# Kernel optimization log

Measured on AMD Instinct MI355X. Metric: run time of the kernel, lower is better.

## Reference

```python
import jax, jax.numpy as jnp
import numpy as np

TAU = 2.0
BN_EPS = 1e-5


def ms_lif(x_seq, v_th):
    # Multi-step LIF: v <- v + (x - v)/tau; spike = H(v - v_th); hard reset to 0.
    def step(v, x):
        v = v + (x - v) / TAU
        s = (v >= v_th).astype(x.dtype)
        v = v * (1.0 - s)
        return v, s
    _, spikes = jax.lax.scan(step, jnp.zeros_like(x_seq[0]), x_seq)
    return spikes


def conv1x1(x, w):
    # x: [TB, C, H, W], w: [O, C]
    return jnp.einsum('bchw,oc->bohw', x, w)


def bn(x, gamma, beta, mean, var):
    scale = gamma / jnp.sqrt(var + BN_EPS)
    shift = beta - mean * scale
    return x * scale[None, :, None, None] + shift[None, :, None, None]


def setup_inputs() -> dict:
    key = jax.random.key(0)
    ks = jax.random.split(key, 20)
    T, B, C, H, W = 4, 32, 384, 16, 16
    d = {'x': jax.random.normal(ks[0], (T, B, C, H, W), jnp.float32)}
    def bn_params(i):
        return (jax.random.uniform(ks[i], (C,), jnp.float32, 0.5, 1.5),
                jax.random.normal(ks[i + 1], (C,), jnp.float32) * 0.1,
                jax.random.normal(ks[i + 2], (C,), jnp.float32) * 0.1,
                jax.random.uniform(ks[i + 3], (C,), jnp.float32, 0.5, 1.5))
    d['q_w'] = jax.random.normal(ks[1], (C, C), jnp.float32) * (C ** -0.5)
    d['q_gamma'], d['q_beta'], d['q_mean'], d['q_var'] = bn_params(2)
    d['k_w'] = jax.random.normal(ks[6], (C, C), jnp.float32) * (C ** -0.5)
    d['k_gamma'], d['k_beta'], d['k_mean'], d['k_var'] = bn_params(7)
    d['v_w'] = jax.random.normal(ks[11], (C, C), jnp.float32) * (C ** -0.5)
    d['v_gamma'], d['v_beta'], d['v_mean'], d['v_var'] = bn_params(12)
    d['proj_w'] = jax.random.normal(ks[16], (C, C), jnp.float32) * (C ** -0.5)
    d['proj_b'] = jnp.zeros((C,), jnp.float32)
    d['proj_gamma'], d['proj_beta'], d['proj_mean'], d['proj_var'] = bn_params(16)
    return d


def reference(x, q_w, q_gamma, q_beta, q_mean, q_var,
              k_w, k_gamma, k_beta, k_mean, k_var,
              v_w, v_gamma, v_beta, v_mean, v_var,
              proj_w, proj_b, proj_gamma, proj_beta, proj_mean, proj_var):
    T, B, C, H, W = x.shape
    nh = 8
    dh = C // nh
    N = H * W
    identity = x
    xs = ms_lif(x, 1.0)                        # shortcut_lif
    xf = xs.reshape(T * B, C, H, W)

    def branch(w, g, b, m, v_):
        y = bn(conv1x1(xf, w), g, b, m, v_).reshape(T, B, C, H, W)
        return ms_lif(y, 1.0)

    def to_heads(s):  # [T,B,C,H,W] -> [T,B,nh,N,dh]
        return s.reshape(T, B, C, N).transpose(0, 1, 3, 2).reshape(T, B, N, nh, dh).transpose(0, 1, 3, 2, 4)

    q = to_heads(branch(q_w, q_gamma, q_beta, q_mean, q_var))
    k = to_heads(branch(k_w, k_gamma, k_beta, k_mean, k_var))
    v = to_heads(branch(v_w, v_gamma, v_beta, v_mean, v_var))

    kv = (k * v).sum(axis=-2, keepdims=True)   # [T,B,nh,1,dh]
    kv = ms_lif(kv, 0.5)                       # talking_heads_lif (v_th=0.5)
    y = q * kv                                 # [T,B,nh,N,dh]
    y = y.transpose(0, 1, 2, 4, 3).reshape(T * B, C, H, W)
    out = conv1x1(y, proj_w) + proj_b[None, :, None, None]
    out = bn(out, proj_gamma, proj_beta, proj_mean, proj_var).reshape(T, B, C, H, W)
    out = out + identity
    return out, v
```

## Files before the change

### kernel.cpp

```cpp
#include <hip/hip_runtime.h>

#define T_ 4
#define B_ 32
#define C_ 384
#define N_ 256
#define NH_ 8
#define DH_ 48
#define CG_ 48
#define WELE_ 147456
#define FRAGS_M_ 442368
#define ELEMS_ ((size_t)T_*B_*C_*N_)

typedef __bf16 bf16x8 __attribute__((ext_vector_type(8)));
typedef float  f32x4  __attribute__((ext_vector_type(4)));
typedef unsigned int u32x4 __attribute__((ext_vector_type(4)));
typedef unsigned int u32x2 __attribute__((ext_vector_type(2)));
typedef unsigned short u16;

__device__ __forceinline__ float bf2f(u16 h){
  unsigned u = ((unsigned)h) << 16;
  return __builtin_bit_cast(float, u);
}
__device__ __forceinline__ u16 f2bf(float f){
  unsigned u = __builtin_bit_cast(unsigned, f);
  u += 0x7FFFu + ((u >> 16) & 1u);
  return (u16)(u >> 16);
}

__global__ __launch_bounds__(256) void k0_split(
    const float* __restrict__ wq, const float* __restrict__ wk,
    const float* __restrict__ wv, const float* __restrict__ wp,
    u16* __restrict__ ws)
{
  const int m = blockIdx.y;
  const int tid = blockIdx.x * 256 + threadIdx.x;
  const float* W = (m == 0) ? wq : (m == 1) ? wk : (m == 2) ? wv : wp;
  const int fo   = tid / 768;
  const int rem  = tid % 768;
  const int k32  = rem / 64;
  const int lane = rem % 64;
  const int row  = fo*16 + (lane & 15);
  const int col  = k32*32 + (lane >> 4)*8;
  const float* src = W + (size_t)row*C_ + col;

  u16 hi8[8], mi8[8], lo8[8];
#pragma unroll
  for (int e = 0; e < 8; e++){
    float w = src[e];
    u16 hi = f2bf(w);  float r1 = w  - bf2f(hi);
    u16 mi = f2bf(r1); float r2 = r1 - bf2f(mi);
    u16 lo = f2bf(r2);
    hi8[e] = hi; mi8[e] = mi; lo8[e] = lo;
  }
  u16* dst = ws + (size_t)m*FRAGS_M_ + (size_t)((fo*12 + k32)*3)*512 + (size_t)lane*8;
  u32x4 pk;
#pragma unroll
  for (int p = 0; p < 3; p++){
    const u16* s = (p == 0) ? hi8 : (p == 1) ? mi8 : lo8;
    pk[0] = (unsigned)s[0] | ((unsigned)s[1] << 16);
    pk[1] = (unsigned)s[2] | ((unsigned)s[3] << 16);
    pk[2] = (unsigned)s[4] | ((unsigned)s[5] << 16);
    pk[3] = (unsigned)s[6] | ((unsigned)s[7] << 16);
    *(u32x4*)(dst + (size_t)p*512) = pk;
  }
}

__global__ __launch_bounds__(256) void k1_lif_in(const float* __restrict__ x, u16* __restrict__ xs)
{
  const int b = blockIdx.x, cg = blockIdx.y, n = threadIdx.x;
  const int c0 = cg * 8;
  float v[8];
#pragma unroll
  for (int i = 0; i < 8; i++) v[i] = 0.f;
#pragma unroll
  for (int t = 0; t < T_; t++){
    const float* xp = x + (((size_t)(t*B_ + b))*C_ + c0)*N_ + n;
    u16 sp[8];
#pragma unroll
    for (int i = 0; i < 8; i++){
      float xv = xp[(size_t)i * N_];
      float vv = v[i] + (xv - v[i]) * 0.5f;
      bool s = vv >= 1.0f;
      sp[i] = s ? (u16)0x3F80u : (u16)0u;
      v[i] = s ? 0.f : vv;
    }
    u32x4 pk;
    pk[0] = (unsigned)sp[0] | ((unsigned)sp[1] << 16);
    pk[1] = (unsigned)sp[2] | ((unsigned)sp[3] << 16);
    pk[2] = (unsigned)sp[4] | ((unsigned)sp[5] << 16);
    pk[3] = (unsigned)sp[6] | ((unsigned)sp[7] << 16);
    *(u32x4*)(xs + ((size_t)((t*B_ + b)*CG_ + cg))*2048 + (size_t)n*8) = pk;
  }
}

__global__ __launch_bounds__(256) void k2_branch(
    const u16* __restrict__ xs, const u16* __restrict__ wsplit,
    const float* __restrict__ gq, const float* __restrict__ beq, const float* __restrict__ mq, const float* __restrict__ vaq,
    const float* __restrict__ gk, const float* __restrict__ bek, const float* __restrict__ mk, const float* __restrict__ vak,
    const float* __restrict__ gv, const float* __restrict__ bev, const float* __restrict__ mv, const float* __restrict__ vav,
    u16* __restrict__ qspk, u16* __restrict__ kspk, u16* __restrict__ vspk)
{
  const int id   = blockIdx.x;
  const int xcd  = id & 7;
  const int rest = id >> 3;
  const int obi  = rest % 18;
  const int nb4  = (rest / 18) & 3;
  const int bloc = rest / 72;
  const int b    = xcd * 4 + bloc;
  const int ob   = obi * 64;
  const int nb   = nb4 * 64;

  const int lane = threadIdx.x & 63;
  const int w = threadIdx.x >> 6;
  const int wo = w & 1, wn = w >> 1;
  const int l15 = lane & 15, lg = lane >> 4;
  const int branch = ob / C_;
  const int obr = (ob % C_) + wo * 32;
  const int fo  = obr >> 4;

  const float *G, *Be, *M, *Va; u16* spdst;
  if (branch == 0){ G=gq; Be=beq; M=mq; Va=vaq; spdst=qspk; }
  else if (branch == 1){ G=gk; Be=bek; M=mk; Va=vak; spdst=kspk; }
  else { G=gv; Be=bev; M=mv; Va=vav; spdst=vspk; }

  const u16* Wb = wsplit + (size_t)branch*FRAGS_M_ + (size_t)lane*8;
  const int nbl = nb + wn * 32;

  const u16* xbt[T_];
#pragma unroll
  for (int t = 0; t < T_; t++)
    xbt[t] = xs + ((size_t)((t*B_ + b)*CG_) + lg)*2048 + (size_t)(nbl + l15)*8;

  f32x4 acc[T_][2][2];
#pragma unroll
  for (int t = 0; t < T_; t++)
#pragma unroll
    for (int io = 0; io < 2; io++)
#pragma unroll
      for (int in = 0; in < 2; in++) acc[t][io][in] = (f32x4){0.f,0.f,0.f,0.f};

  for (int k = 0; k < 12; k++){
    bf16x8 wf[2][3];
#pragma unroll
    for (int io = 0; io < 2; io++)
#pragma unroll
      for (int p = 0; p < 3; p++)
        wf[io][p] = *(const bf16x8*)(Wb + (size_t)(((fo + io)*12 + k)*3 + p)*512);

#pragma unroll
    for (int t = 0; t < T_; t++){
      bf16x8 bb[2];
#pragma unroll
      for (int in = 0; in < 2; in++)
        bb[in] = *(const bf16x8*)(xbt[t] + (size_t)k*8192 + in*128);
#pragma unroll
      for (int in = 0; in < 2; in++){
        acc[t][0][in] = __builtin_amdgcn_mfma_f32_16x16x32_bf16(wf[0][2], bb[in], acc[t][0][in], 0, 0, 0);
        acc[t][0][in] = __builtin_amdgcn_mfma_f32_16x16x32_bf16(wf[0][1], bb[in], acc[t][0][in], 0, 0, 0);
        acc[t][0][in] = __builtin_amdgcn_mfma_f32_16x16x32_bf16(wf[0][0], bb[in], acc[t][0][in], 0, 0, 0);
        acc[t][1][in] = __builtin_amdgcn_mfma_f32_16x16x32_bf16(wf[1][2], bb[in], acc[t][1][in], 0, 0, 0);
        acc[t][1][in] = __builtin_amdgcn_mfma_f32_16x16x32_bf16(wf[1][1], bb[in], acc[t][1][in], 0, 0, 0);
        acc[t][1][in] = __builtin_amdgcn_mfma_f32_16x16x32_bf16(wf[1][0], bb[in], acc[t][1][in], 0, 0, 0);
      }
    }
  }

  float sc[2][4], sh[2][4];
#pragma unroll
  for (int io = 0; io < 2; io++)
#pragma unroll
    for (int j = 0; j < 4; j++){
      int o = obr + io*16 + lg*4 + j;
      float s = G[o] / sqrtf(Va[o] + 1e-5f);
      sc[io][j] = s;
      sh[io][j] = Be[o] - __fmul_rn(M[o], s);
    }

  float vm[2][2][4];
#pragma unroll
  for (int io = 0; io < 2; io++)
#pragma unroll
    for (int in = 0; in < 2; in++)
#pragma unroll
      for (int j = 0; j < 4; j++) vm[io][in][j] = 0.f;

#pragma unroll
  for (int t = 0; t < T_; t++){
#pragma unroll
    for (int io = 0; io < 2; io++)
#pragma unroll
      for (int in = 0; in < 2; in++){
        int n = nbl + in*16 + l15;
        u16 sp[4];
#pragma unroll
        for (int j = 0; j < 4; j++){
          float z = __fadd_rn(__fmul_rn(acc[t][io][in][j], sc[io][j]), sh[io][j]);
          float vv = vm[io][in][j];
          vv = vv + (z - vv) * 0.5f;
          bool s = vv >= 1.0f;
          sp[j] = s ? (u16)0x3F80u : (u16)0u;
          vm[io][in][j] = s ? 0.f : vv;
        }
        u32x2 pk;
        pk[0] = (unsigned)sp[0] | ((unsigned)sp[1] << 16);
        pk[1] = (unsigned)sp[2] | ((unsigned)sp[3] << 16);
        int od = obr + io*16 + lg*4;
        u16* dst = spdst + (size_t)((t*B_ + b)*CG_ + (od >> 3))*2048 + (size_t)n*8 + (od & 7);
        *(u32x2*)dst = pk;
      }
  }
}

__global__ __launch_bounds__(256) void k3_kv(
    const u16* __restrict__ kspk, const u16* __restrict__ vspk, u16* __restrict__ kvm)
{
  const int wid  = (int)((blockIdx.x * blockDim.x + threadIdx.x) >> 6);
  const int lane = threadIdx.x & 63;
  const int b = wid / CG_, cg = wid % CG_;
  float u[8];
#pragma unroll
  for (int i = 0; i < 8; i++) u[i] = 0.f;

#pragma unroll
  for (int t = 0; t < T_; t++){
    int cnt[8];
#pragma unroll
    for (int i = 0; i < 8; i++) cnt[i] = 0;
    const size_t rowoff = (size_t)((t*B_ + b)*CG_ + cg)*2048;
    const u16* kp = kspk + rowoff;
    const u16* vp = vspk + rowoff;
#pragma unroll
    for (int j = 0; j < 4; j++){
      int n = j*64 + lane;
      u32x4 kk = *(const u32x4*)(kp + (size_t)n*8);
      u32x4 vv = *(const u32x4*)(vp + (size_t)n*8);
#pragma unroll
      for (int wd = 0; wd < 4; wd++){
        unsigned both = kk[wd] & vv[wd];
        cnt[2*wd]   += (both & 0xFFFFu) ? 1 : 0;
        cnt[2*wd+1] += (both >> 16)     ? 1 : 0;
      }
    }
#pragma unroll
    for (int i = 0; i < 8; i++){
#pragma unroll
      for (int off = 32; off >= 1; off >>= 1) cnt[i] += __shfl_xor(cnt[i], off, 64);
    }
    u16 mk[8];
#pragma unroll
    for (int i = 0; i < 8; i++){
      float kvf = (float)cnt[i];
      float uu = u[i] + (kvf - u[i]) * 0.5f;
      bool s = uu >= 0.5f;
      mk[i] = s ? (u16)0xFFFFu : (u16)0u;
      u[i] = s ? 0.f : uu;
    }
    if (lane == 0){
      u32x4 pk;
      pk[0] = (unsigned)mk[0] | ((unsigned)mk[1] << 16);
      pk[1] = (unsigned)mk[2] | ((unsigned)mk[3] << 16);
      pk[2] = (unsigned)mk[4] | ((unsigned)mk[5] << 16);
      pk[3] = (unsigned)mk[6] | ((unsigned)mk[7] << 16);
      *(u32x4*)(kvm + (size_t)(t*B_ + b)*C_ + cg*8) = pk;
    }
  }
}

__global__ __launch_bounds__(256) void k5_vtrans(const u16* __restrict__ vspk, float* __restrict__ vout)
{
  const int tb = blockIdx.x, h = blockIdx.y;
  const u16* src = vspk + ((size_t)tb*CG_ + h*6)*2048;
  float* dst = vout + ((size_t)tb*NH_ + h)*(N_*DH_);
#pragma unroll
  for (int i = 0; i < 12; i++){
    int f = i*1024 + threadIdx.x*4;
    int n = f / DH_;
    int d = f - n*DH_;
    u32x2 rv = *(const u32x2*)(src + (size_t)(d >> 3)*2048 + (size_t)n*8 + (d & 7));
    f32x4 o;
    o[0] = (rv[0] & 0xFFFFu) ? 1.f : 0.f;
    o[1] = (rv[0] >> 16)     ? 1.f : 0.f;
    o[2] = (rv[1] & 0xFFFFu) ? 1.f : 0.f;
    o[3] = (rv[1] >> 16)     ? 1.f : 0.f;
    *(f32x4*)(dst + f) = o;
  }
}

__global__ __launch_bounds__(256) void k4_proj(
    const u16* __restrict__ qspk, const u16* __restrict__ kvm, const u16* __restrict__ wsplit,
    const float* __restrict__ pb,
    const float* __restrict__ gp, const float* __restrict__ bep,
    const float* __restrict__ mp, const float* __restrict__ vap,
    const float* __restrict__ x, float* __restrict__ out)
{
  const int id   = blockIdx.x;
  const int xcd  = id & 7;
  const int rest = id >> 3;
  const int obi  = rest % 6;
  const int nb2  = (rest / 6) & 1;
  const int tbl  = rest / 12;
  const int tb   = xcd * 16 + tbl;
  const int ob   = obi * 64;
  const int nb   = nb2 * 128;

  __shared__ __align__(16) u16 kvmask[C_];
  for (int i = threadIdx.x; i < C_; i += 256) kvmask[i] = kvm[(size_t)tb*C_ + i];
  __syncthreads();

  const int lane = threadIdx.x & 63;
  const int w = threadIdx.x >> 6;
  const int wo = w & 1, wn = w >> 1;
  const int l15 = lane & 15, lg = lane >> 4;
  const int obw = ob + wo * 32;
  const int fo  = obw >> 4;
  const int nbl = nb + wn * 64;

  const u16* Wp = wsplit + (size_t)3*FRAGS_M_ + (size_t)lane*8;

  float sc[2][4], sh[2][4], pbv[2][4];
#pragma unroll
  for (int io = 0; io < 2; io++)
#pragma unroll
    for (int j = 0; j < 4; j++){
      int o = obw + io*16 + lg*4 + j;
      float s = gp[o] / sqrtf(vap[o] + 1e-5f);
      sc[io][j] = s;
      sh[io][j] = bep[o] - __fmul_rn(mp[o], s);
      pbv[io][j] = pb[o];
    }

  f32x4 acc[2][4];
#pragma unroll
  for (int io = 0; io < 2; io++)
#pragma unroll
    for (int in = 0; in < 4; in++) acc[io][in] = (f32x4){0.f,0.f,0.f,0.f};

  const u16* qb = qspk + ((size_t)(tb*CG_) + lg)*2048 + (size_t)(nbl + l15)*8;

  for (int k = 0; k < 12; k++){
    bf16x8 a0 = *(const bf16x8*)(Wp + (size_t)(((fo    )*12 + k)*3)*512);
    bf16x8 a1 = *(const bf16x8*)(Wp + (size_t)(((fo + 1)*12 + k)*3)*512);
    u32x4 mv = *(const u32x4*)&kvmask[k*32 + lg*8];
    bf16x8 bb[4];
#pragma unroll
    for (int in = 0; in < 4; in++){
      u32x4 qv = *(const u32x4*)(qb + (size_t)k*8192 + in*128);
      u32x4 yv = qv & mv;
      bb[in] = __builtin_bit_cast(bf16x8, yv);
    }
#pragma unroll
    for (int in = 0; in < 4; in++){
      acc[0][in] = __builtin_amdgcn_mfma_f32_16x16x32_bf16(a0, bb[in], acc[0][in], 0, 0, 0);
      acc[1][in] = __builtin_amdgcn_mfma_f32_16x16x32_bf16(a1, bb[in], acc[1][in], 0, 0, 0);
    }
  }

#pragma unroll
  for (int io = 0; io < 2; io++)
#pragma unroll
    for (int in = 0; in < 4; in++){
      int n = nbl + in*16 + l15;
#pragma unroll
      for (int j = 0; j < 4; j++){
        int o = obw + io*16 + lg*4 + j;
        size_t off = ((size_t)tb*C_ + o)*N_ + n;
        float z = __fadd_rn(acc[io][in][j], pbv[io][j]);
        z = __fmul_rn(z, sc[io][j]);
        z = __fadd_rn(z, sh[io][j]);
        z = __fadd_rn(z, x[off]);
        out[off] = z;
      }
    }
}

extern "C" void kernel_launch(void* const* d_in, const int* in_sizes, int n_in,
                              void* d_out, int out_size, void* d_ws, size_t ws_size,
                              hipStream_t stream)
{
  (void)in_sizes; (void)n_in; (void)out_size; (void)ws_size;
  const float* x   = (const float*)d_in[0];
  const float* qw  = (const float*)d_in[1];
  const float* qg  = (const float*)d_in[2];
  const float* qbe = (const float*)d_in[3];
  const float* qm  = (const float*)d_in[4];
  const float* qva = (const float*)d_in[5];
  const float* kw  = (const float*)d_in[6];
  const float* kg  = (const float*)d_in[7];
  const float* kbe = (const float*)d_in[8];
  const float* km  = (const float*)d_in[9];
  const float* kva = (const float*)d_in[10];
  const float* vw  = (const float*)d_in[11];
  const float* vg  = (const float*)d_in[12];
  const float* vbe = (const float*)d_in[13];
  const float* vm  = (const float*)d_in[14];
  const float* vva = (const float*)d_in[15];
  const float* pw  = (const float*)d_in[16];
  const float* pb  = (const float*)d_in[17];
  const float* pg  = (const float*)d_in[18];
  const float* pbe = (const float*)d_in[19];
  const float* pm  = (const float*)d_in[20];
  const float* pva = (const float*)d_in[21];

  float* out  = (float*)d_out;
  float* vout = out + ELEMS_;

  u16* vspk = (u16*)d_out;

  u16* wsplit = (u16*)d_ws;
  u16* xs   = wsplit + (size_t)4*FRAGS_M_;
  u16* qspk = xs   + ELEMS_;
  u16* kspk = qspk + ELEMS_;
  u16* kvm  = kspk + ELEMS_;

  k0_split<<<dim3(72, 4), 256, 0, stream>>>(qw, kw, vw, pw, wsplit);
  k1_lif_in<<<dim3(B_, CG_), 256, 0, stream>>>(x, xs);
  k2_branch<<<dim3(2304), 256, 0, stream>>>(xs, wsplit,
      qg, qbe, qm, qva,
      kg, kbe, km, kva,
      vg, vbe, vm, vva,
      qspk, kspk, vspk);
  k3_kv<<<dim3(384), 256, 0, stream>>>(kspk, vspk, kvm);
  k5_vtrans<<<dim3(T_*B_, NH_), 256, 0, stream>>>(vspk, vout);
  k4_proj<<<dim3(1536), 256, 0, stream>>>(qspk, kvm, wsplit,
      pb, pg, pbe, pm, pva, x, out);
}
```

Measured before the change: 141.7 us.

## Switch QKV and projection GEMMs to 32x32x16 MFMA tiles

Replaces the 16x16x32 bf16 MFMA tiling with 32x32x16 instructions in the fused QKV conv+BN+LIF kernel and the projection kernel. The weight-splitting kernel writes fragments in the new 32-row layout. Each wave now issues fewer, larger MFMAs and loads fewer activation fragments per K step, which cuts instruction and load overhead. The accumulator register layout changes, so the epilogue index math for BN, LIF and output stores is rewritten, and there is some risk of index errors or different memory access patterns.

```diff
diff --git a/kernel.cpp b/kernel.cpp
--- a/kernel.cpp
+++ b/kernel.cpp
@@ -13,6 +13,7 @@
 
 typedef __bf16 bf16x8 __attribute__((ext_vector_type(8)));
 typedef float  f32x4  __attribute__((ext_vector_type(4)));
+typedef float  f32x16 __attribute__((ext_vector_type(16)));
 typedef unsigned int u32x4 __attribute__((ext_vector_type(4)));
 typedef unsigned int u32x2 __attribute__((ext_vector_type(2)));
 typedef unsigned short u16;
@@ -35,12 +36,12 @@
   const int m = blockIdx.y;
   const int tid = blockIdx.x * 256 + threadIdx.x;
   const float* W = (m == 0) ? wq : (m == 1) ? wk : (m == 2) ? wv : wp;
-  const int fo   = tid / 768;
-  const int rem  = tid % 768;
-  const int k32  = rem / 64;
+  const int fo   = tid / 1536;
+  const int rem  = tid % 1536;
+  const int k16  = rem / 64;
   const int lane = rem % 64;
-  const int row  = fo*16 + (lane & 15);
-  const int col  = k32*32 + (lane >> 4)*8;
+  const int row  = fo*32 + (lane & 31);
+  const int col  = k16*16 + (lane >> 5)*8;
   const float* src = W + (size_t)row*C_ + col;
 
   u16 hi8[8], mi8[8], lo8[8];
@@ -52,7 +53,7 @@
     u16 lo = f2bf(r2);
     hi8[e] = hi; mi8[e] = mi; lo8[e] = lo;
   }
-  u16* dst = ws + (size_t)m*FRAGS_M_ + (size_t)((fo*12 + k32)*3)*512 + (size_t)lane*8;
+  u16* dst = ws + (size_t)m*FRAGS_M_ + (size_t)((fo*24 + k16)*3)*512 + (size_t)lane*8;
   u32x4 pk;
 #pragma unroll
   for (int p = 0; p < 3; p++){
@@ -113,10 +114,10 @@
   const int lane = threadIdx.x & 63;
   const int w = threadIdx.x >> 6;
   const int wo = w & 1, wn = w >> 1;
-  const int l15 = lane & 15, lg = lane >> 4;
+  const int l31 = lane & 31, hi = lane >> 5;
   const int branch = ob / C_;
   const int obr = (ob % C_) + wo * 32;
-  const int fo  = obr >> 4;
+  const int fo  = obr >> 5;
 
   const float *G, *Be, *M, *Va; u16* spdst;
   if (branch == 0){ G=gq; Be=beq; M=mq; Va=vaq; spdst=qspk; }
@@ -125,89 +126,73 @@
 
   const u16* Wb = wsplit + (size_t)branch*FRAGS_M_ + (size_t)lane*8;
   const int nbl = nb + wn * 32;
+  const int n   = nbl + l31;
 
   const u16* xbt[T_];
 #pragma unroll
   for (int t = 0; t < T_; t++)
-    xbt[t] = xs + ((size_t)((t*B_ + b)*CG_) + lg)*2048 + (size_t)(nbl + l15)*8;
-
-  f32x4 acc[T_][2][2];
+    xbt[t] = xs + ((size_t)((t*B_ + b)*CG_) + hi)*2048 + (size_t)n*8;
+
+  f32x16 acc[T_];
 #pragma unroll
   for (int t = 0; t < T_; t++)
 #pragma unroll
-    for (int io = 0; io < 2; io++)
-#pragma unroll
-      for (int in = 0; in < 2; in++) acc[t][io][in] = (f32x4){0.f,0.f,0.f,0.f};
-
-  for (int k = 0; k < 12; k++){
-    bf16x8 wf[2][3];
-#pragma unroll
-    for (int io = 0; io < 2; io++)
-#pragma unroll
-      for (int p = 0; p < 3; p++)
-        wf[io][p] = *(const bf16x8*)(Wb + (size_t)(((fo + io)*12 + k)*3 + p)*512);
+    for (int r = 0; r < 16; r++) acc[t][r] = 0.f;
+
+  for (int k = 0; k < 24; k++){
+    bf16x8 wf[3];
+#pragma unroll
+    for (int p = 0; p < 3; p++)
+      wf[p] = *(const bf16x8*)(Wb + (size_t)((fo*24 + k)*3 + p)*512);
+
+    bf16x8 bb[T_];
+#pragma unroll
+    for (int t = 0; t < T_; t++)
+      bb[t] = *(const bf16x8*)(xbt[t] + (size_t)k*4096);
 
 #pragma unroll
     for (int t = 0; t < T_; t++){
-      bf16x8 bb[2];
-#pragma unroll
-      for (int in = 0; in < 2; in++)
-        bb[in] = *(const bf16x8*)(xbt[t] + (size_t)k*8192 + in*128);
-#pragma unroll
-      for (int in = 0; in < 2; in++){
-        acc[t][0][in] = __builtin_amdgcn_mfma_f32_16x16x32_bf16(wf[0][2], bb[in], acc[t][0][in], 0, 0, 0);
-        acc[t][0][in] = __builtin_amdgcn_mfma_f32_16x16x32_bf16(wf[0][1], bb[in], acc[t][0][in], 0, 0, 0);
-        acc[t][0][in] = __builtin_amdgcn_mfma_f32_16x16x32_bf16(wf[0][0], bb[in], acc[t][0][in], 0, 0, 0);
-        acc[t][1][in] = __builtin_amdgcn_mfma_f32_16x16x32_bf16(wf[1][2], bb[in], acc[t][1][in], 0, 0, 0);
-        acc[t][1][in] = __builtin_amdgcn_mfma_f32_16x16x32_bf16(wf[1][1], bb[in], acc[t][1][in], 0, 0, 0);
-        acc[t][1][in] = __builtin_amdgcn_mfma_f32_16x16x32_bf16(wf[1][0], bb[in], acc[t][1][in], 0, 0, 0);
+      acc[t] = __builtin_amdgcn_mfma_f32_32x32x16_bf16(wf[2], bb[t], acc[t], 0, 0, 0);
+      acc[t] = __builtin_amdgcn_mfma_f32_32x32x16_bf16(wf[1], bb[t], acc[t], 0, 0, 0);
+      acc[t] = __builtin_amdgcn_mfma_f32_32x32x16_bf16(wf[0], bb[t], acc[t], 0, 0, 0);
+    }
+  }
+
+  float sc[16], sh[16];
+#pragma unroll
+  for (int r = 0; r < 16; r++){
+    int o = obr + (r & 3) + 8*(r >> 2) + 4*hi;
+    float s = G[o] / sqrtf(Va[o] + 1e-5f);
+    sc[r] = s;
+    sh[r] = Be[o] - __fmul_rn(M[o], s);
+  }
+
+  float vmr[16];
+#pragma unroll
+  for (int r = 0; r < 16; r++) vmr[r] = 0.f;
+
+#pragma unroll
+  for (int t = 0; t < T_; t++){
+#pragma unroll
+    for (int g = 0; g < 4; g++){
+      u16 sp[4];
+#pragma unroll
+      for (int j = 0; j < 4; j++){
+        int r = g*4 + j;
+        float z = __fadd_rn(__fmul_rn(acc[t][r], sc[r]), sh[r]);
+        float vv = vmr[r];
+        vv = vv + (z - vv) * 0.5f;
+        bool s = vv >= 1.0f;
+        sp[j] = s ? (u16)0x3F80u : (u16)0u;
+        vmr[r] = s ? 0.f : vv;
       }
-    }
-  }
-
-  float sc[2][4], sh[2][4];
-#pragma unroll
-  for (int io = 0; io < 2; io++)
-#pragma unroll
-    for (int j = 0; j < 4; j++){
-      int o = obr + io*16 + lg*4 + j;
-      float s = G[o] / sqrtf(Va[o] + 1e-5f);
-      sc[io][j] = s;
-      sh[io][j] = Be[o] - __fmul_rn(M[o], s);
-    }
-
-  float vm[2][2][4];
-#pragma unroll
-  for (int io = 0; io < 2; io++)
-#pragma unroll
-    for (int in = 0; in < 2; in++)
-#pragma unroll
-      for (int j = 0; j < 4; j++) vm[io][in][j] = 0.f;
-
-#pragma unroll
-  for (int t = 0; t < T_; t++){
-#pragma unroll
-    for (int io = 0; io < 2; io++)
-#pragma unroll
-      for (int in = 0; in < 2; in++){
-        int n = nbl + in*16 + l15;
-        u16 sp[4];
-#pragma unroll
-        for (int j = 0; j < 4; j++){
-          float z = __fadd_rn(__fmul_rn(acc[t][io][in][j], sc[io][j]), sh[io][j]);
-          float vv = vm[io][in][j];
-          vv = vv + (z - vv) * 0.5f;
-          bool s = vv >= 1.0f;
-          sp[j] = s ? (u16)0x3F80u : (u16)0u;
-          vm[io][in][j] = s ? 0.f : vv;
-        }
-        u32x2 pk;
-        pk[0] = (unsigned)sp[0] | ((unsigned)sp[1] << 16);
-        pk[1] = (unsigned)sp[2] | ((unsigned)sp[3] << 16);
-        int od = obr + io*16 + lg*4;
-        u16* dst = spdst + (size_t)((t*B_ + b)*CG_ + (od >> 3))*2048 + (size_t)n*8 + (od & 7);
-        *(u32x2*)dst = pk;
-      }
+      u32x2 pk;
+      pk[0] = (unsigned)sp[0] | ((unsigned)sp[1] << 16);
+      pk[1] = (unsigned)sp[2] | ((unsigned)sp[3] << 16);
+      int od = obr + 8*g + 4*hi;
+      u16* dst = spdst + (size_t)((t*B_ + b)*CG_ + (od >> 3))*2048 + (size_t)n*8 + (od & 7);
+      *(u32x2*)dst = pk;
+    }
   }
 }
 
@@ -310,67 +295,57 @@
   const int lane = threadIdx.x & 63;
   const int w = threadIdx.x >> 6;
   const int wo = w & 1, wn = w >> 1;
-  const int l15 = lane & 15, lg = lane >> 4;
-  const int obw = ob + wo * 32;
-  const int fo  = obw >> 4;
+  const int l31 = lane & 31, hi = lane >> 5;
+  const int ow  = ob + wo * 32;
+  const int fo  = ow >> 5;
   const int nbl = nb + wn * 64;
 
   const u16* Wp = wsplit + (size_t)3*FRAGS_M_ + (size_t)lane*8;
 
-  float sc[2][4], sh[2][4], pbv[2][4];
-#pragma unroll
-  for (int io = 0; io < 2; io++)
-#pragma unroll
-    for (int j = 0; j < 4; j++){
-      int o = obw + io*16 + lg*4 + j;
-      float s = gp[o] / sqrtf(vap[o] + 1e-5f);
-      sc[io][j] = s;
-      sh[io][j] = bep[o] - __fmul_rn(mp[o], s);
-      pbv[io][j] = pb[o];
-    }
-
-  f32x4 acc[2][4];
-#pragma unroll
-  for (int io = 0; io < 2; io++)
-#pragma unroll
-    for (int in = 0; in < 4; in++) acc[io][in] = (f32x4){0.f,0.f,0.f,0.f};
-
-  const u16* qb = qspk + ((size_t)(tb*CG_) + lg)*2048 + (size_t)(nbl + l15)*8;
-
-  for (int k = 0; k < 12; k++){
-    bf16x8 a0 = *(const bf16x8*)(Wp + (size_t)(((fo    )*12 + k)*3)*512);
-    bf16x8 a1 = *(const bf16x8*)(Wp + (size_t)(((fo + 1)*12 + k)*3)*512);
-    u32x4 mv = *(const u32x4*)&kvmask[k*32 + lg*8];
-    bf16x8 bb[4];
-#pragma unroll
-    for (int in = 0; in < 4; in++){
-      u32x4 qv = *(const u32x4*)(qb + (size_t)k*8192 + in*128);
+  float sc[16], sh[16], pbv[16];
+#pragma unroll
+  for (int r = 0; r < 16; r++){
+    int o = ow + (r & 3) + 8*(r >> 2) + 4*hi;
+    float s = gp[o] / sqrtf(vap[o] + 1e-5f);
+    sc[r] = s;
+    sh[r] = bep[o] - __fmul_rn(mp[o], s);
+    pbv[r] = pb[o];
+  }
+
+  f32x16 acc[2];
+#pragma unroll
+  for (int in = 0; in < 2; in++)
+#pragma unroll
+    for (int r = 0; r < 16; r++) acc[in][r] = 0.f;
+
+  const u16* qb = qspk + ((size_t)(tb*CG_) + hi)*2048 + (size_t)(nbl + l31)*8;
+
+  for (int k = 0; k < 24; k++){
+    bf16x8 a = *(const bf16x8*)(Wp + (size_t)((fo*24 + k)*3)*512);
+    u32x4 mv = *(const u32x4*)&kvmask[k*16 + hi*8];
+#pragma unroll
+    for (int in = 0; in < 2; in++){
+      u32x4 qv = *(const u32x4*)(qb + (size_t)k*4096 + in*256);
       u32x4 yv = qv & mv;
-      bb[in] = __builtin_bit_cast(bf16x8, yv);
-    }
-#pragma unroll
-    for (int in = 0; in < 4; in++){
-      acc[0][in] = __builtin_amdgcn_mfma_f32_16x16x32_bf16(a0, bb[in], acc[0][in], 0, 0, 0);
-      acc[1][in] = __builtin_amdgcn_mfma_f32_16x16x32_bf16(a1, bb[in], acc[1][in], 0, 0, 0);
-    }
-  }
-
-#pragma unroll
-  for (int io = 0; io < 2; io++)
-#pragma unroll
-    for (int in = 0; in < 4; in++){
-      int n = nbl + in*16 + l15;
-#pragma unroll
-      for (int j = 0; j < 4; j++){
-        int o = obw + io*16 + lg*4 + j;
-        size_t off = ((size_t)tb*C_ + o)*N_ + n;
-        float z = __fadd_rn(acc[io][in][j], pbv[io][j]);
-        z = __fmul_rn(z, sc[io][j]);
-        z = __fadd_rn(z, sh[io][j]);
-        z = __fadd_rn(z, x[off]);
-        out[off] = z;
-      }
-    }
+      bf16x8 bbv = __builtin_bit_cast(bf16x8, yv);
+      acc[in] = __builtin_amdgcn_mfma_f32_32x32x16_bf16(a, bbv, acc[in], 0, 0, 0);
+    }
+  }
+
+#pragma unroll
+  for (int in = 0; in < 2; in++){
+    int n = nbl + in*32 + l31;
+#pragma unroll
+    for (int r = 0; r < 16; r++){
+      int o = ow + (r & 3) + 8*(r >> 2) + 4*hi;
+      size_t off = ((size_t)tb*C_ + o)*N_ + n;
+      float z = __fadd_rn(acc[in][r], pbv[r]);
+      z = __fmul_rn(z, sc[r]);
+      z = __fadd_rn(z, sh[r]);
+      z = __fadd_rn(z, x[off]);
+      out[off] = z;
+    }
+  }
 }
 
 extern "C" void kernel_launch(void* const* d_in, const int* in_sizes, int n_in,
```

After: 206.7 us. 45.9% more time.

## Drop low bf16 weight split and recompute near-threshold spikes exactly

Applied to the files above, without the earlier changes.

The branch GEMM now uses only the hi and mid bf16 parts of the weights, cutting MFMA count and weight loads by a third. A per-row bound on the dropped residual flags outputs whose LIF membrane lands near the threshold; those are queued via an atomic list and recomputed exactly in fp32 by a new fix-up kernel. The weight split and input LIF kernels are also merged into one launch that computes the residual bounds. This adds atomics, a serial fix pass, and a capacity limit on the list that could miss corrections if exceeded.

```diff
diff --git a/kernel.cpp b/kernel.cpp
--- a/kernel.cpp
+++ b/kernel.cpp
@@ -10,6 +10,7 @@
 #define WELE_ 147456
 #define FRAGS_M_ 442368
 #define ELEMS_ ((size_t)T_*B_*C_*N_)
+#define FIXCAP_ 262144u
 
 typedef __bf16 bf16x8 __attribute__((ext_vector_type(8)));
 typedef float  f32x4  __attribute__((ext_vector_type(4)));
@@ -27,69 +28,86 @@
   return (u16)(u >> 16);
 }
 
-__global__ __launch_bounds__(256) void k0_split(
+__global__ __launch_bounds__(256) void k01_prep(
+    const float* __restrict__ x,
     const float* __restrict__ wq, const float* __restrict__ wk,
     const float* __restrict__ wv, const float* __restrict__ wp,
-    u16* __restrict__ ws)
-{
-  const int m = blockIdx.y;
-  const int tid = blockIdx.x * 256 + threadIdx.x;
-  const float* W = (m == 0) ? wq : (m == 1) ? wk : (m == 2) ? wv : wp;
-  const int fo   = tid / 768;
-  const int rem  = tid % 768;
-  const int k32  = rem / 64;
-  const int lane = rem % 64;
-  const int row  = fo*16 + (lane & 15);
-  const int col  = k32*32 + (lane >> 4)*8;
-  const float* src = W + (size_t)row*C_ + col;
-
-  u16 hi8[8], mi8[8], lo8[8];
-#pragma unroll
-  for (int e = 0; e < 8; e++){
-    float w = src[e];
-    u16 hi = f2bf(w);  float r1 = w  - bf2f(hi);
-    u16 mi = f2bf(r1); float r2 = r1 - bf2f(mi);
-    u16 lo = f2bf(r2);
-    hi8[e] = hi; mi8[e] = mi; lo8[e] = lo;
-  }
-  u16* dst = ws + (size_t)m*FRAGS_M_ + (size_t)((fo*12 + k32)*3)*512 + (size_t)lane*8;
-  u32x4 pk;
-#pragma unroll
-  for (int p = 0; p < 3; p++){
-    const u16* s = (p == 0) ? hi8 : (p == 1) ? mi8 : lo8;
-    pk[0] = (unsigned)s[0] | ((unsigned)s[1] << 16);
-    pk[1] = (unsigned)s[2] | ((unsigned)s[3] << 16);
-    pk[2] = (unsigned)s[4] | ((unsigned)s[5] << 16);
-    pk[3] = (unsigned)s[6] | ((unsigned)s[7] << 16);
-    *(u32x4*)(dst + (size_t)p*512) = pk;
-  }
-}
-
-__global__ __launch_bounds__(256) void k1_lif_in(const float* __restrict__ x, u16* __restrict__ xs)
-{
-  const int b = blockIdx.x, cg = blockIdx.y, n = threadIdx.x;
-  const int c0 = cg * 8;
-  float v[8];
-#pragma unroll
-  for (int i = 0; i < 8; i++) v[i] = 0.f;
-#pragma unroll
-  for (int t = 0; t < T_; t++){
-    const float* xp = x + (((size_t)(t*B_ + b))*C_ + c0)*N_ + n;
-    u16 sp[8];
-#pragma unroll
-    for (int i = 0; i < 8; i++){
-      float xv = xp[(size_t)i * N_];
-      float vv = v[i] + (xv - v[i]) * 0.5f;
-      bool s = vv >= 1.0f;
-      sp[i] = s ? (u16)0x3F80u : (u16)0u;
-      v[i] = s ? 0.f : vv;
-    }
+    u16* __restrict__ ws, u16* __restrict__ xs,
+    float* __restrict__ R2, unsigned* __restrict__ cnt)
+{
+  const int blk = blockIdx.x;
+  if (blk < 288){
+    const int m = blk / 72;
+    const int tid = (blk % 72) * 256 + threadIdx.x;
+    const float* W = (m == 0) ? wq : (m == 1) ? wk : (m == 2) ? wv : wp;
+    const int fo   = tid / 768;
+    const int rem  = tid % 768;
+    const int k32  = rem / 64;
+    const int lane = rem % 64;
+    const int row  = fo*16 + (lane & 15);
+    const int col  = k32*32 + (lane >> 4)*8;
+    const float* src = W + (size_t)row*C_ + col;
+
+    u16 hi8[8], mi8[8], lo8[8];
+#pragma unroll
+    for (int e = 0; e < 8; e++){
+      float w = src[e];
+      u16 hi = f2bf(w);  float r1 = w  - bf2f(hi);
+      u16 mi = f2bf(r1); float r2 = r1 - bf2f(mi);
+      u16 lo = f2bf(r2);
+      hi8[e] = hi; mi8[e] = mi; lo8[e] = lo;
+    }
+    u16* dst = ws + (size_t)m*FRAGS_M_ + (size_t)((fo*12 + k32)*3)*512 + (size_t)lane*8;
     u32x4 pk;
-    pk[0] = (unsigned)sp[0] | ((unsigned)sp[1] << 16);
-    pk[1] = (unsigned)sp[2] | ((unsigned)sp[3] << 16);
-    pk[2] = (unsigned)sp[4] | ((unsigned)sp[5] << 16);
-    pk[3] = (unsigned)sp[6] | ((unsigned)sp[7] << 16);
-    *(u32x4*)(xs + ((size_t)((t*B_ + b)*CG_ + cg))*2048 + (size_t)n*8) = pk;
+#pragma unroll
+    for (int p = 0; p < 3; p++){
+      const u16* s = (p == 0) ? hi8 : (p == 1) ? mi8 : lo8;
+      pk[0] = (unsigned)s[0] | ((unsigned)s[1] << 16);
+      pk[1] = (unsigned)s[2] | ((unsigned)s[3] << 16);
+      pk[2] = (unsigned)s[4] | ((unsigned)s[5] << 16);
+      pk[3] = (unsigned)s[6] | ((unsigned)s[7] << 16);
+      *(u32x4*)(dst + (size_t)p*512) = pk;
+    }
+  } else if (blk < 1824){
+    const int bid = blk - 288;
+    const int b = bid / CG_, cg = bid % CG_;
+    const int n = threadIdx.x;
+    const int c0 = cg * 8;
+    float v[8];
+#pragma unroll
+    for (int i = 0; i < 8; i++) v[i] = 0.f;
+#pragma unroll
+    for (int t = 0; t < T_; t++){
+      const float* xp = x + (((size_t)(t*B_ + b))*C_ + c0)*N_ + n;
+      u16 sp[8];
+#pragma unroll
+      for (int i = 0; i < 8; i++){
+        float xv = xp[(size_t)i * N_];
+        float vv = v[i] + (xv - v[i]) * 0.5f;
+        bool s = vv >= 1.0f;
+        sp[i] = s ? (u16)0x3F80u : (u16)0u;
+        v[i] = s ? 0.f : vv;
+      }
+      u32x4 pk;
+      pk[0] = (unsigned)sp[0] | ((unsigned)sp[1] << 16);
+      pk[1] = (unsigned)sp[2] | ((unsigned)sp[3] << 16);
+      pk[2] = (unsigned)sp[4] | ((unsigned)sp[5] << 16);
+      pk[3] = (unsigned)sp[6] | ((unsigned)sp[7] << 16);
+      *(u32x4*)(xs + ((size_t)((t*B_ + b)*CG_ + cg))*2048 + (size_t)n*8) = pk;
+    }
+  } else {
+    if (blk == 1824 && threadIdx.x == 0) *cnt = 0u;
+    const int tid = (blk - 1824) * 256 + threadIdx.x;
+    const int m = tid / 384, o = tid % 384;
+    const float* Wr = ((m == 0) ? wq : (m == 1) ? wk : (m == 2) ? wv : wp) + (size_t)o*C_;
+    float s = 0.f;
+    for (int c = 0; c < C_; c++){
+      float w = Wr[c];
+      u16 hi = f2bf(w);  float r1 = w  - bf2f(hi);
+      u16 mi = f2bf(r1); float r2 = r1 - bf2f(mi);
+      s += fabsf(r2);
+    }
+    R2[tid] = s;
   }
 }
 
@@ -98,6 +116,7 @@
     const float* __restrict__ gq, const float* __restrict__ beq, const float* __restrict__ mq, const float* __restrict__ vaq,
     const float* __restrict__ gk, const float* __restrict__ bek, const float* __restrict__ mk, const float* __restrict__ vak,
     const float* __restrict__ gv, const float* __restrict__ bev, const float* __restrict__ mv, const float* __restrict__ vav,
+    const float* __restrict__ R2, unsigned* __restrict__ cnt, unsigned* __restrict__ list,
     u16* __restrict__ qspk, u16* __restrict__ kspk, u16* __restrict__ vspk)
 {
   const int id   = blockIdx.x;
@@ -122,6 +141,7 @@
   if (branch == 0){ G=gq; Be=beq; M=mq; Va=vaq; spdst=qspk; }
   else if (branch == 1){ G=gk; Be=bek; M=mk; Va=vak; spdst=kspk; }
   else { G=gv; Be=bev; M=mv; Va=vav; spdst=vspk; }
+  const float* R2b = R2 + branch*C_;
 
   const u16* Wb = wsplit + (size_t)branch*FRAGS_M_ + (size_t)lane*8;
   const int nbl = nb + wn * 32;
@@ -140,12 +160,12 @@
       for (int in = 0; in < 2; in++) acc[t][io][in] = (f32x4){0.f,0.f,0.f,0.f};
 
   for (int k = 0; k < 12; k++){
-    bf16x8 wf[2][3];
-#pragma unroll
-    for (int io = 0; io < 2; io++)
-#pragma unroll
-      for (int p = 0; p < 3; p++)
-        wf[io][p] = *(const bf16x8*)(Wb + (size_t)(((fo + io)*12 + k)*3 + p)*512);
+    bf16x8 wf[2][2];
+#pragma unroll
+    for (int io = 0; io < 2; io++){
+      wf[io][0] = *(const bf16x8*)(Wb + (size_t)(((fo + io)*12 + k)*3 + 0)*512);
+      wf[io][1] = *(const bf16x8*)(Wb + (size_t)(((fo + io)*12 + k)*3 + 1)*512);
+    }
 
 #pragma unroll
     for (int t = 0; t < T_; t++){
@@ -155,17 +175,15 @@
         bb[in] = *(const bf16x8*)(xbt[t] + (size_t)k*8192 + in*128);
 #pragma unroll
       for (int in = 0; in < 2; in++){
-        acc[t][0][in] = __builtin_amdgcn_mfma_f32_16x16x32_bf16(wf[0][2], bb[in], acc[t][0][in], 0, 0, 0);
         acc[t][0][in] = __builtin_amdgcn_mfma_f32_16x16x32_bf16(wf[0][1], bb[in], acc[t][0][in], 0, 0, 0);
         acc[t][0][in] = __builtin_amdgcn_mfma_f32_16x16x32_bf16(wf[0][0], bb[in], acc[t][0][in], 0, 0, 0);
-        acc[t][1][in] = __builtin_amdgcn_mfma_f32_16x16x32_bf16(wf[1][2], bb[in], acc[t][1][in], 0, 0, 0);
         acc[t][1][in] = __builtin_amdgcn_mfma_f32_16x16x32_bf16(wf[1][1], bb[in], acc[t][1][in], 0, 0, 0);
         acc[t][1][in] = __builtin_amdgcn_mfma_f32_16x16x32_bf16(wf[1][0], bb[in], acc[t][1][in], 0, 0, 0);
       }
     }
   }
 
-  float sc[2][4], sh[2][4];
+  float sc[2][4], sh[2][4], eps[2][4];
 #pragma unroll
   for (int io = 0; io < 2; io++)
 #pragma unroll
@@ -174,6 +192,7 @@
       float s = G[o] / sqrtf(Va[o] + 1e-5f);
       sc[io][j] = s;
       sh[io][j] = Be[o] - __fmul_rn(M[o], s);
+      eps[io][j] = 1.5f * fabsf(s) * R2b[o] + 1e-5f;
     }
 
   float vm[2][2][4];
@@ -184,6 +203,7 @@
 #pragma unroll
       for (int j = 0; j < 4; j++) vm[io][in][j] = 0.f;
 
+  unsigned flagm = 0;
 #pragma unroll
   for (int t = 0; t < T_; t++){
 #pragma unroll
@@ -198,6 +218,7 @@
           float vv = vm[io][in][j];
           vv = vv + (z - vv) * 0.5f;
           bool s = vv >= 1.0f;
+          if (fabsf(vv - 1.0f) < eps[io][j]) flagm |= 1u << ((io*2 + in)*4 + j);
           sp[j] = s ? (u16)0x3F80u : (u16)0u;
           vm[io][in][j] = s ? 0.f : vv;
         }
@@ -209,6 +230,74 @@
         *(u32x2*)dst = pk;
       }
   }
+
+  if (flagm){
+#pragma unroll
+    for (int io = 0; io < 2; io++)
+#pragma unroll
+      for (int in = 0; in < 2; in++)
+#pragma unroll
+        for (int j = 0; j < 4; j++)
+          if (flagm & (1u << ((io*2 + in)*4 + j))){
+            unsigned idx = atomicAdd(cnt, 1u);
+            if (idx < FIXCAP_){
+              int o  = obr + io*16 + lg*4 + j;
+              int og = branch*C_ + o;
+              int n  = nbl + in*16 + l15;
+              list[idx] = (unsigned)n | ((unsigned)b << 8) | ((unsigned)og << 13);
+            }
+          }
+  }
+}
+
+__global__ __launch_bounds__(256) void k2_fix(
+    const unsigned* __restrict__ cnt, const unsigned* __restrict__ list,
+    const u16* __restrict__ xs,
+    const float* __restrict__ wq, const float* __restrict__ wk, const float* __restrict__ wv,
+    const float* __restrict__ gq, const float* __restrict__ beq, const float* __restrict__ mq, const float* __restrict__ vaq,
+    const float* __restrict__ gk, const float* __restrict__ bek, const float* __restrict__ mk, const float* __restrict__ vak,
+    const float* __restrict__ gv, const float* __restrict__ bev, const float* __restrict__ mv, const float* __restrict__ vav,
+    u16* __restrict__ qspk, u16* __restrict__ kspk, u16* __restrict__ vspk)
+{
+  unsigned total = *cnt;
+  if (total > FIXCAP_) total = FIXCAP_;
+  for (unsigned idx = blockIdx.x*256 + threadIdx.x; idx < total; idx += gridDim.x*256){
+    unsigned e = list[idx];
+    int n = (int)(e & 255u);
+    int b = (int)((e >> 8) & 31u);
+    int og = (int)(e >> 13);
+    int branch = og / C_, o = og % C_;
+    const float *Wr, *G, *Be, *M, *Va; u16* spdst;
+    if (branch == 0){ Wr=wq; G=gq; Be=beq; M=mq; Va=vaq; spdst=qspk; }
+    else if (branch == 1){ Wr=wk; G=gk; Be=bek; M=mk; Va=vak; spdst=kspk; }
+    else { Wr=wv; G=gv; Be=bev; M=mv; Va=vav; spdst=vspk; }
+    Wr += (size_t)o*C_;
+    float s2 = G[o] / sqrtf(Va[o] + 1e-5f);
+    float sh = Be[o] - __fmul_rn(M[o], s2);
+    float v = 0.f;
+#pragma unroll
+    for (int t = 0; t < T_; t++){
+      const u16* sp = xs + (size_t)((t*B_ + b)*CG_)*2048 + (size_t)n*8;
+      float z = 0.f;
+      for (int cg = 0; cg < CG_; cg++){
+        u32x4 kv = *(const u32x4*)(sp + (size_t)cg*2048);
+        const float* wr = Wr + cg*8;
+        z += (kv[0] & 0xFFFFu) ? wr[0] : 0.f;
+        z += (kv[0] >> 16)     ? wr[1] : 0.f;
+        z += (kv[1] & 0xFFFFu) ? wr[2] : 0.f;
+        z += (kv[1] >> 16)     ? wr[3] : 0.f;
+        z += (kv[2] & 0xFFFFu) ? wr[4] : 0.f;
+        z += (kv[2] >> 16)     ? wr[5] : 0.f;
+        z += (kv[3] & 0xFFFFu) ? wr[6] : 0.f;
+        z += (kv[3] >> 16)     ? wr[7] : 0.f;
+      }
+      float zb = __fadd_rn(__fmul_rn(z, s2), sh);
+      float vv = v + (zb - v) * 0.5f;
+      bool s = vv >= 1.0f;
+      spdst[(size_t)((t*B_ + b)*CG_ + (o >> 3))*2048 + (size_t)n*8 + (o & 7)] = s ? (u16)0x3F80u : (u16)0u;
+      v = s ? 0.f : vv;
+    }
+  }
 }
 
 __global__ __launch_bounds__(256) void k3_kv(
@@ -223,9 +312,9 @@
 
 #pragma unroll
   for (int t = 0; t < T_; t++){
-    int cnt[8];
-#pragma unroll
-    for (int i = 0; i < 8; i++) cnt[i] = 0;
+    int cnt_[8];
+#pragma unroll
+    for (int i = 0; i < 8; i++) cnt_[i] = 0;
     const size_t rowoff = (size_t)((t*B_ + b)*CG_ + cg)*2048;
     const u16* kp = kspk + rowoff;
     const u16* vp = vspk + rowoff;
@@ -237,19 +326,19 @@
 #pragma unroll
       for (int wd = 0; wd < 4; wd++){
         unsigned both = kk[wd] & vv[wd];
-        cnt[2*wd]   += (both & 0xFFFFu) ? 1 : 0;
-        cnt[2*wd+1] += (both >> 16)     ? 1 : 0;
+        cnt_[2*wd]   += (both & 0xFFFFu) ? 1 : 0;
+        cnt_[2*wd+1] += (both >> 16)     ? 1 : 0;
       }
     }
 #pragma unroll
     for (int i = 0; i < 8; i++){
 #pragma unroll
-      for (int off = 32; off >= 1; off >>= 1) cnt[i] += __shfl_xor(cnt[i], off, 64);
+      for (int off = 32; off >= 1; off >>= 1) cnt_[i] += __shfl_xor(cnt_[i], off, 64);
     }
     u16 mk[8];
 #pragma unroll
     for (int i = 0; i < 8; i++){
-      float kvf = (float)cnt[i];
+      float kvf = (float)cnt_[i];
       float uu = u[i] + (kvf - u[i]) * 0.5f;
       bool s = uu >= 0.5f;
       mk[i] = s ? (u16)0xFFFFu : (u16)0u;
@@ -411,16 +500,25 @@
   u16* qspk = xs   + ELEMS_;
   u16* kspk = qspk + ELEMS_;
   u16* kvm  = kspk + ELEMS_;
-
-  k0_split<<<dim3(72, 4), 256, 0, stream>>>(qw, kw, vw, pw, wsplit);
-  k1_lif_in<<<dim3(B_, CG_), 256, 0, stream>>>(x, xs);
+  float*    R2   = (float*)(kvm + 49152);
+  unsigned* cntp = (unsigned*)(R2 + 1536);
+  unsigned* list = cntp + 4;
+
+  k01_prep<<<dim3(1830), 256, 0, stream>>>(x, qw, kw, vw, pw, wsplit, xs, R2, cntp);
   k2_branch<<<dim3(2304), 256, 0, stream>>>(xs, wsplit,
       qg, qbe, qm, qva,
       kg, kbe, km, kva,
       vg, vbe, vm, vva,
+      R2, cntp, list,
       qspk, kspk, vspk);
+  k2_fix<<<dim3(64), 256, 0, stream>>>(cntp, list, xs,
+      qw, kw, vw,
+      qg, qbe, qm, qva,
+      kg, kbe, km, kva,
+      vg, vbe, vm, vva,
+      qspk, kspk, vspk);
+  k5_vtrans<<<dim3(T_*B_, NH_), 256, 0, stream>>>(vspk, vout);
   k3_kv<<<dim3(384), 256, 0, stream>>>(kspk, vspk, kvm);
-  k5_vtrans<<<dim3(T_*B_, NH_), 256, 0, stream>>>(vspk, vout);
   k4_proj<<<dim3(1536), 256, 0, stream>>>(qspk, kvm, wsplit,
       pb, pg, pbe, pm, pva, x, out);
 }
```

After: 161.3 us. +13.9%, slower.
